# Optimization experiments

Measured on AMD Instinct MI355X. Metric: run time of the kernel, lower is better.

## Reference

```python
import jax, jax.numpy as jnp
import numpy as np

N = 8388608
EPS = 1e-12  # matches torch eps default


def setup_inputs() -> dict:
    key = jax.random.key(0)
    k1, k2, k3 = jax.random.split(key, 3)
    logits = jax.random.normal(k1, (N,), dtype=jnp.float32)
    status = jax.random.randint(k2, (N,), 0, 2, dtype=jnp.int32)       # 0=censored, 1=event
    time = jax.random.randint(k3, (N,), 0, 65536, dtype=jnp.int32)     # integer survival times -> ties
    return {"logits": logits, "status": status, "time": time}


def reference(logits, status, time):
    """Cox partial likelihood, Breslow tie correction, reduction='mean'.

    Per the torch module: sort by time descending, cum_exp = cumsum(exp(x)),
    for each tie group with m events: nll = -(sum_events x - m*log(cum_exp[group_end]+eps)).
    This equals sum over events of -(x_i - log(denom_i)) with denom_i shared per group,
    which vectorizes cleanly.
    """
    neg_t = -time                       # ascending key == descending time order
    order = jnp.argsort(neg_t)
    x = logits[order]
    e = status[order].astype(x.dtype)
    t = neg_t[order]                    # sorted ascending (i.e., time descending)
    exp_x = jnp.exp(x)
    cum_exp = jnp.cumsum(exp_x)
    # last index of each tie group (risk-set boundary), vectorized unique_consecutive
    ends = jnp.searchsorted(t, t, side='right') - 1
    denom = cum_exp[ends] + EPS
    nll = (jnp.log(denom) - x) * e      # contributes only at events
    n_events = e.sum()
    return nll.sum() / (n_events + EPS)
```

## Files before the change

### kernel.cpp

```cpp
#include <hip/hip_runtime.h>
#include <math.h>

#define NBUCKETS 65536
#define EPS 1e-12

typedef float v4f __attribute__((ext_vector_type(4)));
typedef int v4i __attribute__((ext_vector_type(4)));
typedef unsigned int v4u __attribute__((ext_vector_type(4)));

#define NCHUNK 128
#define WGT 1024
#define RROUNDS 16
#define PBUCK 32768
#define SCALE_F 131072.0f
#define INV_SCALE (1.0 / 131072.0)
#define SUM_MASK 0x0FFFFFFFu

#define OFF_HIST 0
#define OFF_CS   (NCHUNK * NBUCKETS * 4)
#define OFF_SX   (OFF_CS + 256 * 8)
#define OFF_CTRL (OFF_SX + NCHUNK * 4)
#define REQ_NEW  (OFF_CTRL + 64)

#define NREP 8
#define OSCALE_F 1073741824.0f
#define OINV_SCALE (1.0 / 1073741824.0)
#define LOW48 ((1ull << 48) - 1)
#define O_REP 0
#define O_SD (NREP * NBUCKETS * 8)
#define O_M (O_SD + NBUCKETS * 8)
#define O_CS (O_M + NBUCKETS * 4)
#define O_NLL (O_CS + 256 * 8)
#define O_NEV (O_NLL + 256 * 8)
#define O_SX (O_NEV + 256 * 4)
#define REQ_OLD (O_SX + 8192 * 4)

__device__ __forceinline__ unsigned int xcd_id() {
    unsigned int x;
    asm volatile("s_getreg_b32 %0, hwreg(HW_REG_XCC_ID)" : "=s"(x));
    return x & 7u;
}

__global__ __launch_bounds__(WGT) void scatter_half_kernel(
        const v4f* __restrict__ x4, const v4i* __restrict__ e4,
        const v4i* __restrict__ t4, unsigned int* __restrict__ hist,
        float* __restrict__ sum_ex_part, unsigned int* __restrict__ ctrl, int n4,
        const float* __restrict__ x_s, const int* __restrict__ e_s,
        const int* __restrict__ t_s, int tail_base, int tail_cnt) {
    __shared__ unsigned int lds[PBUCK];
    const int t = threadIdx.x;
    const int wg = blockIdx.x;
    const int half = wg & 1;
    const int chunk = wg >> 1;

    if (wg == 0 && t == 0) {
        ctrl[0] = 0u;
        ctrl[1] = 0u;
        ((double*)ctrl)[1] = 0.0;
        ctrl[4] = 0u;
    }

    v4u* lds4 = (v4u*)lds;
#pragma unroll
    for (int q = 0; q < PBUCK / 4 / WGT; q++)
        lds4[t + q * WGT] = (v4u){0u, 0u, 0u, 0u};
    __syncthreads();

    float ev_x = 0.0f;
    const unsigned int uh = (unsigned int)half;

#pragma unroll 1
    for (int r = 0; r < RROUNDS; r++) {
        int idx = (chunk * RROUNDS + r) * WGT + t;
        if (idx < n4) {
            v4f x = __builtin_nontemporal_load(&x4[idx]);
            v4i e = __builtin_nontemporal_load(&e4[idx]);
            v4i tm = __builtin_nontemporal_load(&t4[idx]);
#pragma unroll
            for (int k = 0; k < 4; k++) {
                float xv = x[k];
                unsigned int b = (unsigned int)tm[k] & 0xFFFFu;
                unsigned int ev = (e[k] != 0) ? 1u : 0u;
                if ((b >> 15) == uh) {
                    unsigned int pk = (ev << 28) +
                                      (unsigned int)(expf(xv) * SCALE_F + 0.5f);
                    atomicAdd(&lds[b & (PBUCK - 1)], pk);
                }
                if (half == 0 && ev) ev_x += xv;
            }
        }
    }

    if (chunk == 0 && t == 0 && tail_cnt > 0) {
        for (int i = 0; i < tail_cnt; i++) {
            int idx = tail_base + i;
            float xv = x_s[idx];
            unsigned int b = (unsigned int)t_s[idx] & 0xFFFFu;
            unsigned int ev = (e_s[idx] != 0) ? 1u : 0u;
            if ((b >> 15) == uh) {
                unsigned int pk = (ev << 28) +
                                  (unsigned int)(expf(xv) * SCALE_F + 0.5f);
                atomicAdd(&lds[b & (PBUCK - 1)], pk);
            }
            if (half == 0 && ev) ev_x += xv;
        }
    }
    __syncthreads();

    v4u* hbase = (v4u*)(hist + (size_t)chunk * NBUCKETS + (size_t)half * PBUCK);
#pragma unroll
    for (int q = 0; q < PBUCK / 4 / WGT; q++) {
        v4u v = lds4[t + q * WGT];
        __builtin_nontemporal_store(v, &hbase[t + q * WGT]);
    }

    if (half == 0) {
        __syncthreads();
#pragma unroll
        for (int off = 32; off > 0; off >>= 1) ev_x += __shfl_down(ev_x, off, 64);
        if ((t & 63) == 0) lds[t >> 6] = __float_as_uint(ev_x);
        __syncthreads();
        if (t == 0) {
            float s = 0.0f;
            for (int w = 0; w < WGT / 64; w++) s += __uint_as_float(lds[w]);
            sum_ex_part[chunk] = s;
        }
    }
}

__global__ __launch_bounds__(256) void merge_suffix_final_kernel(
        const v4u* __restrict__ hist4, double* __restrict__ chunk_sum,
        const float* __restrict__ sum_ex_part, unsigned int* __restrict__ ctrl,
        float* __restrict__ out) {
    const int t = threadIdx.x, b = blockIdx.x;
    const int tg = t >> 6, lane = t & 63;

    unsigned long long s[4] = {0ull, 0ull, 0ull, 0ull};
    unsigned int c[4] = {0u, 0u, 0u, 0u};
    const v4u* base = hist4 + (size_t)(tg * (NCHUNK / 4)) * (NBUCKETS / 4) +
                      (size_t)b * 64 + lane;
#pragma unroll 4
    for (int w = 0; w < NCHUNK / 4; w++) {
        v4u h = base[(size_t)w * (NBUCKETS / 4)];
#pragma unroll
        for (int q = 0; q < 4; q++) {
            s[q] += (unsigned long long)(h[q] & SUM_MASK);
            c[q] += h[q] >> 28;
        }
    }
    __shared__ unsigned long long lsum[4][64][4];
    __shared__ unsigned int lcnt[4][64][4];
#pragma unroll
    for (int q = 0; q < 4; q++) { lsum[tg][lane][q] = s[q]; lcnt[tg][lane][q] = c[q]; }
    __syncthreads();

    unsigned long long Ssum = lsum[0][t >> 2][t & 3] + lsum[1][t >> 2][t & 3] +
                              lsum[2][t >> 2][t & 3] + lsum[3][t >> 2][t & 3];
    unsigned int M = lcnt[0][t >> 2][t & 3] + lcnt[1][t >> 2][t & 3] +
                     lcnt[2][t >> 2][t & 3] + lcnt[3][t >> 2][t & 3];
    double sv = (double)Ssum * INV_SCALE;

    __shared__ double red[256];
    __shared__ double sfx[256];
    __shared__ unsigned int ured[256];
    __shared__ int lastblk;

    red[t] = sv;
    __syncthreads();
    for (int st = 128; st > 0; st >>= 1) {
        if (t < st) red[t] += red[t + st];
        __syncthreads();
    }
    if (t == 0) {
        __hip_atomic_store(&chunk_sum[b], red[0], __ATOMIC_RELEASE,
                           __HIP_MEMORY_SCOPE_AGENT);
        __hip_atomic_fetch_add(&ctrl[0], 1u, __ATOMIC_ACQ_REL,
                               __HIP_MEMORY_SCOPE_AGENT);
        while (__hip_atomic_load(&ctrl[0], __ATOMIC_ACQUIRE,
                                 __HIP_MEMORY_SCOPE_AGENT) < (unsigned)gridDim.x)
            __builtin_amdgcn_s_sleep(8);
    }
    __syncthreads();

    double cst = __hip_atomic_load(&chunk_sum[t], __ATOMIC_RELAXED,
                                   __HIP_MEMORY_SCOPE_AGENT);
    red[t] = (t > b) ? cst : 0.0;
    __syncthreads();
    for (int st = 128; st > 0; st >>= 1) {
        if (t < st) red[t] += red[t + st];
        __syncthreads();
    }
    double offset = red[0];
    __syncthreads();

    sfx[t] = sv;
    __syncthreads();
    for (int st = 1; st < 256; st <<= 1) {
        double add = (t + st < 256) ? sfx[t + st] : 0.0;
        __syncthreads();
        sfx[t] += add;
        __syncthreads();
    }
    double denom = offset + sfx[t] + EPS;
    double nll = (M != 0u) ? (double)M * log(denom) : 0.0;

    red[t] = nll;
    ured[t] = M;
    __syncthreads();
    for (int st = 128; st > 0; st >>= 1) {
        if (t < st) { red[t] += red[t + st]; ured[t] += ured[t + st]; }
        __syncthreads();
    }
    if (t == 0) {
        atomicAdd((double*)ctrl + 1, red[0]);
        atomicAdd(&ctrl[4], ured[0]);
        __threadfence();
        unsigned int old = __hip_atomic_fetch_add(&ctrl[1], 1u, __ATOMIC_ACQ_REL,
                                                  __HIP_MEMORY_SCOPE_AGENT);
        lastblk = (old == (unsigned)gridDim.x - 1) ? 1 : 0;
    }
    __syncthreads();
    if (lastblk) {
        red[t] = (t < NCHUNK) ? (double)sum_ex_part[t] : 0.0;
        __syncthreads();
        for (int st = 128; st > 0; st >>= 1) {
            if (t < st) red[t] += red[t + st];
            __syncthreads();
        }
        if (t == 0) {
            double nllT = __hip_atomic_load((double*)ctrl + 1, __ATOMIC_RELAXED,
                                            __HIP_MEMORY_SCOPE_AGENT);
            unsigned int nev = __hip_atomic_load(&ctrl[4], __ATOMIC_RELAXED,
                                                 __HIP_MEMORY_SCOPE_AGENT);
            out[0] = (float)((nllT - red[0]) / ((double)nev + EPS));
        }
    }
}

__global__ void zero_ws_kernel(unsigned long long* __restrict__ rep, int n) {
    int i = blockIdx.x * blockDim.x + threadIdx.x;
    if (i < n) rep[i] = 0ull;
}

__global__ __launch_bounds__(256) void scatter_atomic_kernel(
        const v4f* __restrict__ x4, const v4i* __restrict__ e4,
        const v4i* __restrict__ t4,
        unsigned long long* __restrict__ rep, float* __restrict__ sum_ex_part,
        int n4, const float* __restrict__ x_s, const int* __restrict__ e_s,
        const int* __restrict__ t_s, int tail_base, int tail_cnt) {
    int i = blockIdx.x * blockDim.x + threadIdx.x;
    unsigned long long* R = rep + (size_t)xcd_id() * NBUCKETS;
    float ev_x = 0.0f;
    if (i < n4) {
        v4f x = __builtin_nontemporal_load(&x4[i]);
        v4i e = __builtin_nontemporal_load(&e4[i]);
        v4i t = __builtin_nontemporal_load(&t4[i]);
#pragma unroll
        for (int k = 0; k < 4; k++) {
            float xv = x[k];
            unsigned int v = (unsigned int)t[k] & 0xFFFFu;
            unsigned long long pk =
                ((unsigned long long)(e[k] != 0) << 48) +
                (unsigned long long)(expf(xv) * OSCALE_F + 0.5f);
            __hip_atomic_fetch_add(&R[v], pk, __ATOMIC_RELAXED,
                                   __HIP_MEMORY_SCOPE_WORKGROUP);
            if (e[k]) ev_x += xv;
        }
    }
    if (i < tail_cnt) {
        int idx = tail_base + i;
        float xv = x_s[idx];
        unsigned int v = (unsigned int)t_s[idx] & 0xFFFFu;
        unsigned long long pk =
            ((unsigned long long)(e_s[idx] != 0) << 48) +
            (unsigned long long)(expf(xv) * OSCALE_F + 0.5f);
        __hip_atomic_fetch_add(&R[v], pk, __ATOMIC_RELAXED,
                               __HIP_MEMORY_SCOPE_WORKGROUP);
        if (e_s[idx]) ev_x += xv;
    }
    __shared__ float sred[256];
    sred[threadIdx.x] = ev_x;
    __syncthreads();
    for (int s = 128; s > 0; s >>= 1) {
        if ((int)threadIdx.x < s) sred[threadIdx.x] += sred[threadIdx.x + s];
        __syncthreads();
    }
    if (threadIdx.x == 0) sum_ex_part[blockIdx.x] = sred[0];
}

__global__ __launch_bounds__(256) void reduce_kernel(
        const unsigned long long* __restrict__ rep, double* __restrict__ Sd,
        unsigned int* __restrict__ m, double* __restrict__ chunk_sum) {
    int t = threadIdx.x;
    int i = blockIdx.x * 256 + t;
    unsigned long long acc = 0ull;
#pragma unroll
    for (int r = 0; r < NREP; r++) acc += rep[(size_t)r * NBUCKETS + i];
    double sv = (double)(acc & LOW48) * OINV_SCALE;
    unsigned int mv = (unsigned int)(acc >> 48);
    Sd[i] = sv;
    m[i] = mv;
    __shared__ double red[256];
    red[t] = sv;
    __syncthreads();
    for (int s = 128; s > 0; s >>= 1) {
        if (t < s) red[t] += red[t + s];
        __syncthreads();
    }
    if (t == 0) chunk_sum[blockIdx.x] = red[0];
}

__global__ __launch_bounds__(256) void suffix_kernel(
        const double* __restrict__ Sd, const unsigned int* __restrict__ m,
        const double* __restrict__ chunk_sum, double* __restrict__ nll_part,
        unsigned int* __restrict__ nev_part) {
    __shared__ double cs[256];
    __shared__ double sfx[256];
    __shared__ unsigned int ured[256];
    const int t = threadIdx.x;
    const int b = blockIdx.x;

    cs[t] = (t > b) ? chunk_sum[t] : 0.0;
    __syncthreads();
    for (int s = 128; s > 0; s >>= 1) {
        if (t < s) cs[t] += cs[t + s];
        __syncthreads();
    }
    double offset = cs[0];
    __syncthreads();

    int i = b * 256 + t;
    double sv = Sd[i];
    unsigned int mv = m[i];

    sfx[t] = sv;
    __syncthreads();
    for (int s = 1; s < 256; s <<= 1) {
        double add = (t + s < 256) ? sfx[t + s] : 0.0;
        __syncthreads();
        sfx[t] += add;
        __syncthreads();
    }

    double denom = offset + sfx[t] + EPS;
    double nll = (mv != 0u) ? (double)mv * log(denom) : 0.0;

    cs[t] = nll;
    ured[t] = mv;
    __syncthreads();
    for (int s = 128; s > 0; s >>= 1) {
        if (t < s) { cs[t] += cs[t + s]; ured[t] += ured[t + s]; }
        __syncthreads();
    }
    if (t == 0) {
        nll_part[b] = cs[0];
        nev_part[b] = ured[0];
    }
}

__global__ __launch_bounds__(256) void final_kernel(
        const double* __restrict__ nll_part, const unsigned int* __restrict__ nev_part,
        const float* __restrict__ sum_ex_part, int n_sx, float* __restrict__ out) {
    __shared__ double rd[256];
    __shared__ double rs[256];
    __shared__ unsigned int ru[256];
    int t = threadIdx.x;
    double nll = nll_part[t];
    unsigned int ne = nev_part[t];
    double sx = 0.0;
    for (int i = t; i < n_sx; i += 256) sx += (double)sum_ex_part[i];
    rd[t] = nll;
    rs[t] = sx;
    ru[t] = ne;
    __syncthreads();
    for (int s = 128; s > 0; s >>= 1) {
        if (t < s) { rd[t] += rd[t + s]; rs[t] += rs[t + s]; ru[t] += ru[t + s]; }
        __syncthreads();
    }
    if (t == 0) {
        double total = rd[0] - rs[0];
        out[0] = (float)(total / ((double)ru[0] + EPS));
    }
}

extern "C" void kernel_launch(void* const* d_in, const int* in_sizes, int n_in,
                              void* d_out, int out_size, void* d_ws, size_t ws_size,
                              hipStream_t stream) {
    const float* logits = (const float*)d_in[0];
    const int* status = (const int*)d_in[1];
    const int* time = (const int*)d_in[2];
    const int N = in_sizes[0];

    char* ws = (char*)d_ws;
    int n4 = N / 4;
    int tail_base = n4 * 4;
    int tail_cnt = N - tail_base;

    if (ws_size >= (size_t)REQ_NEW && N <= NCHUNK * WGT * RROUNDS * 4) {
        unsigned int* hist = (unsigned int*)(ws + OFF_HIST);
        double* chunk_sum = (double*)(ws + OFF_CS);
        float* sum_ex_part = (float*)(ws + OFF_SX);
        unsigned int* ctrl = (unsigned int*)(ws + OFF_CTRL);

        scatter_half_kernel<<<NCHUNK * 2, WGT, 0, stream>>>(
            (const v4f*)logits, (const v4i*)status, (const v4i*)time,
            hist, sum_ex_part, ctrl, n4, logits, status, time, tail_base, tail_cnt);
        merge_suffix_final_kernel<<<256, 256, 0, stream>>>(
            (const v4u*)hist, chunk_sum, sum_ex_part, ctrl, (float*)d_out);
    } else {
        unsigned long long* rep = (unsigned long long*)(ws + O_REP);
        double* Sd = (double*)(ws + O_SD);
        unsigned int* m = (unsigned int*)(ws + O_M);
        double* chunk_sum = (double*)(ws + O_CS);
        double* nll_part = (double*)(ws + O_NLL);
        unsigned int* nev_part = (unsigned int*)(ws + O_NEV);
        float* sum_ex_part = (float*)(ws + O_SX);

        int nrep_total = NREP * NBUCKETS;
        zero_ws_kernel<<<(nrep_total + 255) / 256, 256, 0, stream>>>(rep, nrep_total);
        int blocks = (n4 + 255) / 256;
        if (blocks < 1) blocks = 1;
        scatter_atomic_kernel<<<blocks, 256, 0, stream>>>(
            (const v4f*)logits, (const v4i*)status, (const v4i*)time,
            rep, sum_ex_part, n4, logits, status, time, tail_base, tail_cnt);
        reduce_kernel<<<256, 256, 0, stream>>>(rep, Sd, m, chunk_sum);
        suffix_kernel<<<256, 256, 0, stream>>>(Sd, m, chunk_sum, nll_part, nev_part);
        final_kernel<<<1, 256, 0, stream>>>(nll_part, nev_part, sum_ex_part, blocks,
                                            (float*)d_out);
    }
}
```

Baseline: 175.8 us.

## Split fused merge/suffix kernel into separate launches instead of grid-wide spin barrier

Replaces the single merge_suffix_final kernel, which used an atomic spin barrier across all blocks plus last-block detection, with three launches: merge_chunk, suffix and final. Per-bucket sums and counts now go to global workspace arrays, and the existing suffix and final kernels are reused. This drops the in-kernel grid barrier and atomic control words, but adds two kernel launches and extra global round trips.

```diff
diff --git a/kernel.cpp b/kernel.cpp
--- a/kernel.cpp
+++ b/kernel.cpp
@@ -17,10 +17,13 @@
 #define SUM_MASK 0x0FFFFFFFu
 
 #define OFF_HIST 0
-#define OFF_CS   (NCHUNK * NBUCKETS * 4)
-#define OFF_SX   (OFF_CS + 256 * 8)
-#define OFF_CTRL (OFF_SX + NCHUNK * 4)
-#define REQ_NEW  (OFF_CTRL + 64)
+#define OFF_SD   (NCHUNK * NBUCKETS * 4)
+#define OFF_M    (OFF_SD + NBUCKETS * 8)
+#define OFF_CS   (OFF_M + NBUCKETS * 4)
+#define OFF_NLL  (OFF_CS + 256 * 8)
+#define OFF_NEV  (OFF_NLL + 256 * 8)
+#define OFF_SX   (OFF_NEV + 256 * 4)
+#define REQ_NEW  (OFF_SX + NCHUNK * 4)
 
 #define NREP 8
 #define OSCALE_F 1073741824.0f
@@ -44,7 +47,7 @@
 __global__ __launch_bounds__(WGT) void scatter_half_kernel(
         const v4f* __restrict__ x4, const v4i* __restrict__ e4,
         const v4i* __restrict__ t4, unsigned int* __restrict__ hist,
-        float* __restrict__ sum_ex_part, unsigned int* __restrict__ ctrl, int n4,
+        float* __restrict__ sum_ex_part, int n4,
         const float* __restrict__ x_s, const int* __restrict__ e_s,
         const int* __restrict__ t_s, int tail_base, int tail_cnt) {
     __shared__ unsigned int lds[PBUCK];
@@ -52,13 +55,6 @@
     const int wg = blockIdx.x;
     const int half = wg & 1;
     const int chunk = wg >> 1;
-
-    if (wg == 0 && t == 0) {
-        ctrl[0] = 0u;
-        ctrl[1] = 0u;
-        ((double*)ctrl)[1] = 0.0;
-        ctrl[4] = 0u;
-    }
 
     v4u* lds4 = (v4u*)lds;
 #pragma unroll
@@ -128,10 +124,9 @@
     }
 }
 
-__global__ __launch_bounds__(256) void merge_suffix_final_kernel(
-        const v4u* __restrict__ hist4, double* __restrict__ chunk_sum,
-        const float* __restrict__ sum_ex_part, unsigned int* __restrict__ ctrl,
-        float* __restrict__ out) {
+__global__ __launch_bounds__(256) void merge_chunk_kernel(
+        const v4u* __restrict__ hist4, double* __restrict__ Sd,
+        unsigned int* __restrict__ m, double* __restrict__ chunk_sum) {
     const int t = threadIdx.x, b = blockIdx.x;
     const int tg = t >> 6, lane = t & 63;
 
@@ -159,155 +154,17 @@
     unsigned int M = lcnt[0][t >> 2][t & 3] + lcnt[1][t >> 2][t & 3] +
                      lcnt[2][t >> 2][t & 3] + lcnt[3][t >> 2][t & 3];
     double sv = (double)Ssum * INV_SCALE;
+    Sd[b * 256 + t] = sv;
+    m[b * 256 + t] = M;
 
     __shared__ double red[256];
-    __shared__ double sfx[256];
-    __shared__ unsigned int ured[256];
-    __shared__ int lastblk;
-
     red[t] = sv;
     __syncthreads();
     for (int st = 128; st > 0; st >>= 1) {
         if (t < st) red[t] += red[t + st];
         __syncthreads();
     }
-    if (t == 0) {
-        __hip_atomic_store(&chunk_sum[b], red[0], __ATOMIC_RELEASE,
-                           __HIP_MEMORY_SCOPE_AGENT);
-        __hip_atomic_fetch_add(&ctrl[0], 1u, __ATOMIC_ACQ_REL,
-                               __HIP_MEMORY_SCOPE_AGENT);
-        while (__hip_atomic_load(&ctrl[0], __ATOMIC_ACQUIRE,
-                                 __HIP_MEMORY_SCOPE_AGENT) < (unsigned)gridDim.x)
-            __builtin_amdgcn_s_sleep(8);
-    }
-    __syncthreads();
-
-    double cst = __hip_atomic_load(&chunk_sum[t], __ATOMIC_RELAXED,
-                                   __HIP_MEMORY_SCOPE_AGENT);
-    red[t] = (t > b) ? cst : 0.0;
-    __syncthreads();
-    for (int st = 128; st > 0; st >>= 1) {
-        if (t < st) red[t] += red[t + st];
-        __syncthreads();
-    }
-    double offset = red[0];
-    __syncthreads();
-
-    sfx[t] = sv;
-    __syncthreads();
-    for (int st = 1; st < 256; st <<= 1) {
-        double add = (t + st < 256) ? sfx[t + st] : 0.0;
-        __syncthreads();
-        sfx[t] += add;
-        __syncthreads();
-    }
-    double denom = offset + sfx[t] + EPS;
-    double nll = (M != 0u) ? (double)M * log(denom) : 0.0;
-
-    red[t] = nll;
-    ured[t] = M;
-    __syncthreads();
-    for (int st = 128; st > 0; st >>= 1) {
-        if (t < st) { red[t] += red[t + st]; ured[t] += ured[t + st]; }
-        __syncthreads();
-    }
-    if (t == 0) {
-        atomicAdd((double*)ctrl + 1, red[0]);
-        atomicAdd(&ctrl[4], ured[0]);
-        __threadfence();
-        unsigned int old = __hip_atomic_fetch_add(&ctrl[1], 1u, __ATOMIC_ACQ_REL,
-                                                  __HIP_MEMORY_SCOPE_AGENT);
-        lastblk = (old == (unsigned)gridDim.x - 1) ? 1 : 0;
-    }
-    __syncthreads();
-    if (lastblk) {
-        red[t] = (t < NCHUNK) ? (double)sum_ex_part[t] : 0.0;
-        __syncthreads();
-        for (int st = 128; st > 0; st >>= 1) {
-            if (t < st) red[t] += red[t + st];
-            __syncthreads();
-        }
-        if (t == 0) {
-            double nllT = __hip_atomic_load((double*)ctrl + 1, __ATOMIC_RELAXED,
-                                            __HIP_MEMORY_SCOPE_AGENT);
-            unsigned int nev = __hip_atomic_load(&ctrl[4], __ATOMIC_RELAXED,
-                                                 __HIP_MEMORY_SCOPE_AGENT);
-            out[0] = (float)((nllT - red[0]) / ((double)nev + EPS));
-        }
-    }
-}
-
-__global__ void zero_ws_kernel(unsigned long long* __restrict__ rep, int n) {
-    int i = blockIdx.x * blockDim.x + threadIdx.x;
-    if (i < n) rep[i] = 0ull;
-}
-
-__global__ __launch_bounds__(256) void scatter_atomic_kernel(
-        const v4f* __restrict__ x4, const v4i* __restrict__ e4,
-        const v4i* __restrict__ t4,
-        unsigned long long* __restrict__ rep, float* __restrict__ sum_ex_part,
-        int n4, const float* __restrict__ x_s, const int* __restrict__ e_s,
-        const int* __restrict__ t_s, int tail_base, int tail_cnt) {
-    int i = blockIdx.x * blockDim.x + threadIdx.x;
-    unsigned long long* R = rep + (size_t)xcd_id() * NBUCKETS;
-    float ev_x = 0.0f;
-    if (i < n4) {
-        v4f x = __builtin_nontemporal_load(&x4[i]);
-        v4i e = __builtin_nontemporal_load(&e4[i]);
-        v4i t = __builtin_nontemporal_load(&t4[i]);
-#pragma unroll
-        for (int k = 0; k < 4; k++) {
-            float xv = x[k];
-            unsigned int v = (unsigned int)t[k] & 0xFFFFu;
-            unsigned long long pk =
-                ((unsigned long long)(e[k] != 0) << 48) +
-                (unsigned long long)(expf(xv) * OSCALE_F + 0.5f);
-            __hip_atomic_fetch_add(&R[v], pk, __ATOMIC_RELAXED,
-                                   __HIP_MEMORY_SCOPE_WORKGROUP);
-            if (e[k]) ev_x += xv;
-        }
-    }
-    if (i < tail_cnt) {
-        int idx = tail_base + i;
-        float xv = x_s[idx];
-        unsigned int v = (unsigned int)t_s[idx] & 0xFFFFu;
-        unsigned long long pk =
-            ((unsigned long long)(e_s[idx] != 0) << 48) +
-            (unsigned long long)(expf(xv) * OSCALE_F + 0.5f);
-        __hip_atomic_fetch_add(&R[v], pk, __ATOMIC_RELAXED,
-                               __HIP_MEMORY_SCOPE_WORKGROUP);
-        if (e_s[idx]) ev_x += xv;
-    }
-    __shared__ float sred[256];
-    sred[threadIdx.x] = ev_x;
-    __syncthreads();
-    for (int s = 128; s > 0; s >>= 1) {
-        if ((int)threadIdx.x < s) sred[threadIdx.x] += sred[threadIdx.x + s];
-        __syncthreads();
-    }
-    if (threadIdx.x == 0) sum_ex_part[blockIdx.x] = sred[0];
-}
-
-__global__ __launch_bounds__(256) void reduce_kernel(
-        const unsigned long long* __restrict__ rep, double* __restrict__ Sd,
-        unsigned int* __restrict__ m, double* __restrict__ chunk_sum) {
-    int t = threadIdx.x;
-    int i = blockIdx.x * 256 + t;
-    unsigned long long acc = 0ull;
-#pragma unroll
-    for (int r = 0; r < NREP; r++) acc += rep[(size_t)r * NBUCKETS + i];
-    double sv = (double)(acc & LOW48) * OINV_SCALE;
-    unsigned int mv = (unsigned int)(acc >> 48);
-    Sd[i] = sv;
-    m[i] = mv;
-    __shared__ double red[256];
-    red[t] = sv;
-    __syncthreads();
-    for (int s = 128; s > 0; s >>= 1) {
-        if (t < s) red[t] += red[t + s];
-        __syncthreads();
-    }
-    if (t == 0) chunk_sum[blockIdx.x] = red[0];
+    if (t == 0) chunk_sum[b] = red[0];
 }
 
 __global__ __launch_bounds__(256) void suffix_kernel(
@@ -383,6 +240,79 @@
     }
 }
 
+__global__ void zero_ws_kernel(unsigned long long* __restrict__ rep, int n) {
+    int i = blockIdx.x * blockDim.x + threadIdx.x;
+    if (i < n) rep[i] = 0ull;
+}
+
+__global__ __launch_bounds__(256) void scatter_atomic_kernel(
+        const v4f* __restrict__ x4, const v4i* __restrict__ e4,
+        const v4i* __restrict__ t4,
+        unsigned long long* __restrict__ rep, float* __restrict__ sum_ex_part,
+        int n4, const float* __restrict__ x_s, const int* __restrict__ e_s,
+        const int* __restrict__ t_s, int tail_base, int tail_cnt) {
+    int i = blockIdx.x * blockDim.x + threadIdx.x;
+    unsigned long long* R = rep + (size_t)xcd_id() * NBUCKETS;
+    float ev_x = 0.0f;
+    if (i < n4) {
+        v4f x = __builtin_nontemporal_load(&x4[i]);
+        v4i e = __builtin_nontemporal_load(&e4[i]);
+        v4i t = __builtin_nontemporal_load(&t4[i]);
+#pragma unroll
+        for (int k = 0; k < 4; k++) {
+            float xv = x[k];
+            unsigned int v = (unsigned int)t[k] & 0xFFFFu;
+            unsigned long long pk =
+                ((unsigned long long)(e[k] != 0) << 48) +
+                (unsigned long long)(expf(xv) * OSCALE_F + 0.5f);
+            __hip_atomic_fetch_add(&R[v], pk, __ATOMIC_RELAXED,
+                                   __HIP_MEMORY_SCOPE_WORKGROUP);
+            if (e[k]) ev_x += xv;
+        }
+    }
+    if (i < tail_cnt) {
+        int idx = tail_base + i;
+        float xv = x_s[idx];
+        unsigned int v = (unsigned int)t_s[idx] & 0xFFFFu;
+        unsigned long long pk =
+            ((unsigned long long)(e_s[idx] != 0) << 48) +
+            (unsigned long long)(expf(xv) * OSCALE_F + 0.5f);
+        __hip_atomic_fetch_add(&R[v], pk, __ATOMIC_RELAXED,
+                               __HIP_MEMORY_SCOPE_WORKGROUP);
+        if (e_s[idx]) ev_x += xv;
+    }
+    __shared__ float sred[256];
+    sred[threadIdx.x] = ev_x;
+    __syncthreads();
+    for (int s = 128; s > 0; s >>= 1) {
+        if ((int)threadIdx.x < s) sred[threadIdx.x] += sred[threadIdx.x + s];
+        __syncthreads();
+    }
+    if (threadIdx.x == 0) sum_ex_part[blockIdx.x] = sred[0];
+}
+
+__global__ __launch_bounds__(256) void reduce_kernel(
+        const unsigned long long* __restrict__ rep, double* __restrict__ Sd,
+        unsigned int* __restrict__ m, double* __restrict__ chunk_sum) {
+    int t = threadIdx.x;
+    int i = blockIdx.x * 256 + t;
+    unsigned long long acc = 0ull;
+#pragma unroll
+    for (int r = 0; r < NREP; r++) acc += rep[(size_t)r * NBUCKETS + i];
+    double sv = (double)(acc & LOW48) * OINV_SCALE;
+    unsigned int mv = (unsigned int)(acc >> 48);
+    Sd[i] = sv;
+    m[i] = mv;
+    __shared__ double red[256];
+    red[t] = sv;
+    __syncthreads();
+    for (int s = 128; s > 0; s >>= 1) {
+        if (t < s) red[t] += red[t + s];
+        __syncthreads();
+    }
+    if (t == 0) chunk_sum[blockIdx.x] = red[0];
+}
+
 extern "C" void kernel_launch(void* const* d_in, const int* in_sizes, int n_in,
                               void* d_out, int out_size, void* d_ws, size_t ws_size,
                               hipStream_t stream) {
@@ -398,15 +328,20 @@
 
     if (ws_size >= (size_t)REQ_NEW && N <= NCHUNK * WGT * RROUNDS * 4) {
         unsigned int* hist = (unsigned int*)(ws + OFF_HIST);
+        double* Sd = (double*)(ws + OFF_SD);
+        unsigned int* m = (unsigned int*)(ws + OFF_M);
         double* chunk_sum = (double*)(ws + OFF_CS);
+        double* nll_part = (double*)(ws + OFF_NLL);
+        unsigned int* nev_part = (unsigned int*)(ws + OFF_NEV);
         float* sum_ex_part = (float*)(ws + OFF_SX);
-        unsigned int* ctrl = (unsigned int*)(ws + OFF_CTRL);
 
         scatter_half_kernel<<<NCHUNK * 2, WGT, 0, stream>>>(
             (const v4f*)logits, (const v4i*)status, (const v4i*)time,
-            hist, sum_ex_part, ctrl, n4, logits, status, time, tail_base, tail_cnt);
-        merge_suffix_final_kernel<<<256, 256, 0, stream>>>(
-            (const v4u*)hist, chunk_sum, sum_ex_part, ctrl, (float*)d_out);
+            hist, sum_ex_part, n4, logits, status, time, tail_base, tail_cnt);
+        merge_chunk_kernel<<<256, 256, 0, stream>>>((const v4u*)hist, Sd, m, chunk_sum);
+        suffix_kernel<<<256, 256, 0, stream>>>(Sd, m, chunk_sum, nll_part, nev_part);
+        final_kernel<<<1, 256, 0, stream>>>(nll_part, nev_part, sum_ex_part, NCHUNK,
+                                            (float*)d_out);
     } else {
         unsigned long long* rep = (unsigned long long*)(ws + O_REP);
         double* Sd = (double*)(ws + O_SD);
```

Result: faster. 154.2 us (-12.3%).

## Split merge kernel at grid barrier and drop nontemporal input loads

Applied to the files above, without the earlier changes.

Replaces the in-kernel spin-wait grid barrier in the merge/suffix kernel with a kernel boundary. A merge_chunk kernel now writes per-bucket sums, event counts and chunk totals to workspace, and a separate suffix_final kernel computes the suffix scan and the final loss. It also changes the input loads in both scatter kernels from nontemporal to ordinary loads. This removes the spinning wait on the atomic counter and the need for all 256 blocks to be co-resident, at the cost of an extra launch and a 768 KB round-trip through global memory for the bucket data.

```diff
diff --git a/kernel.cpp b/kernel.cpp
--- a/kernel.cpp
+++ b/kernel.cpp
@@ -17,7 +17,9 @@
 #define SUM_MASK 0x0FFFFFFFu
 
 #define OFF_HIST 0
-#define OFF_CS   (NCHUNK * NBUCKETS * 4)
+#define OFF_SD   (NCHUNK * NBUCKETS * 4)
+#define OFF_M    (OFF_SD + NBUCKETS * 8)
+#define OFF_CS   (OFF_M + NBUCKETS * 4)
 #define OFF_SX   (OFF_CS + 256 * 8)
 #define OFF_CTRL (OFF_SX + NCHUNK * 4)
 #define REQ_NEW  (OFF_CTRL + 64)
@@ -44,7 +46,7 @@
 __global__ __launch_bounds__(WGT) void scatter_half_kernel(
         const v4f* __restrict__ x4, const v4i* __restrict__ e4,
         const v4i* __restrict__ t4, unsigned int* __restrict__ hist,
-        float* __restrict__ sum_ex_part, unsigned int* __restrict__ ctrl, int n4,
+        float* __restrict__ sum_ex_part, int n4,
         const float* __restrict__ x_s, const int* __restrict__ e_s,
         const int* __restrict__ t_s, int tail_base, int tail_cnt) {
     __shared__ unsigned int lds[PBUCK];
@@ -52,13 +54,7 @@
     const int wg = blockIdx.x;
     const int half = wg & 1;
     const int chunk = wg >> 1;
-
-    if (wg == 0 && t == 0) {
-        ctrl[0] = 0u;
-        ctrl[1] = 0u;
-        ((double*)ctrl)[1] = 0.0;
-        ctrl[4] = 0u;
-    }
+    const unsigned int uh = (unsigned int)half;
 
     v4u* lds4 = (v4u*)lds;
 #pragma unroll
@@ -67,15 +63,14 @@
     __syncthreads();
 
     float ev_x = 0.0f;
-    const unsigned int uh = (unsigned int)half;
 
 #pragma unroll 1
     for (int r = 0; r < RROUNDS; r++) {
         int idx = (chunk * RROUNDS + r) * WGT + t;
         if (idx < n4) {
-            v4f x = __builtin_nontemporal_load(&x4[idx]);
-            v4i e = __builtin_nontemporal_load(&e4[idx]);
-            v4i tm = __builtin_nontemporal_load(&t4[idx]);
+            v4f x = x4[idx];
+            v4i e = e4[idx];
+            v4i tm = t4[idx];
 #pragma unroll
             for (int k = 0; k < 4; k++) {
                 float xv = x[k];
@@ -128,12 +123,18 @@
     }
 }
 
-__global__ __launch_bounds__(256) void merge_suffix_final_kernel(
-        const v4u* __restrict__ hist4, double* __restrict__ chunk_sum,
-        const float* __restrict__ sum_ex_part, unsigned int* __restrict__ ctrl,
-        float* __restrict__ out) {
+__global__ __launch_bounds__(256) void merge_chunk_kernel(
+        const v4u* __restrict__ hist4, double* __restrict__ Sd,
+        unsigned int* __restrict__ m, double* __restrict__ chunk_sum,
+        unsigned int* __restrict__ ctrl) {
     const int t = threadIdx.x, b = blockIdx.x;
     const int tg = t >> 6, lane = t & 63;
+
+    if (b == 0 && t == 0) {
+        ctrl[0] = 0u;
+        ((double*)ctrl)[1] = 0.0;
+        ctrl[4] = 0u;
+    }
 
     unsigned long long s[4] = {0ull, 0ull, 0ull, 0ull};
     unsigned int c[4] = {0u, 0u, 0u, 0u};
@@ -159,72 +160,76 @@
     unsigned int M = lcnt[0][t >> 2][t & 3] + lcnt[1][t >> 2][t & 3] +
                      lcnt[2][t >> 2][t & 3] + lcnt[3][t >> 2][t & 3];
     double sv = (double)Ssum * INV_SCALE;
+    Sd[b * 256 + t] = sv;
+    m[b * 256 + t] = M;
 
     __shared__ double red[256];
+    red[t] = sv;
+    __syncthreads();
+    for (int st = 128; st > 0; st >>= 1) {
+        if (t < st) red[t] += red[t + st];
+        __syncthreads();
+    }
+    if (t == 0) chunk_sum[b] = red[0];
+}
+
+__global__ __launch_bounds__(256) void suffix_final_kernel(
+        const double* __restrict__ Sd, const unsigned int* __restrict__ m,
+        const double* __restrict__ chunk_sum, const float* __restrict__ sum_ex_part,
+        unsigned int* __restrict__ ctrl, float* __restrict__ out) {
+    __shared__ double cs[256];
     __shared__ double sfx[256];
     __shared__ unsigned int ured[256];
     __shared__ int lastblk;
-
-    red[t] = sv;
-    __syncthreads();
-    for (int st = 128; st > 0; st >>= 1) {
-        if (t < st) red[t] += red[t + st];
+    const int t = threadIdx.x;
+    const int b = blockIdx.x;
+
+    cs[t] = (t > b) ? chunk_sum[t] : 0.0;
+    __syncthreads();
+    for (int s = 128; s > 0; s >>= 1) {
+        if (t < s) cs[t] += cs[t + s];
+        __syncthreads();
+    }
+    double offset = cs[0];
+    __syncthreads();
+
+    int i = b * 256 + t;
+    double sv = Sd[i];
+    unsigned int mv = m[i];
+
+    sfx[t] = sv;
+    __syncthreads();
+    for (int s = 1; s < 256; s <<= 1) {
+        double add = (t + s < 256) ? sfx[t + s] : 0.0;
+        __syncthreads();
+        sfx[t] += add;
+        __syncthreads();
+    }
+
+    double denom = offset + sfx[t] + EPS;
+    double nll = (mv != 0u) ? (double)mv * log(denom) : 0.0;
+
+    cs[t] = nll;
+    ured[t] = mv;
+    __syncthreads();
+    for (int s = 128; s > 0; s >>= 1) {
+        if (t < s) { cs[t] += cs[t + s]; ured[t] += ured[t + s]; }
         __syncthreads();
     }
     if (t == 0) {
-        __hip_atomic_store(&chunk_sum[b], red[0], __ATOMIC_RELEASE,
-                           __HIP_MEMORY_SCOPE_AGENT);
-        __hip_atomic_fetch_add(&ctrl[0], 1u, __ATOMIC_ACQ_REL,
-                               __HIP_MEMORY_SCOPE_AGENT);
-        while (__hip_atomic_load(&ctrl[0], __ATOMIC_ACQUIRE,
-                                 __HIP_MEMORY_SCOPE_AGENT) < (unsigned)gridDim.x)
-            __builtin_amdgcn_s_sleep(8);
-    }
-    __syncthreads();
-
-    double cst = __hip_atomic_load(&chunk_sum[t], __ATOMIC_RELAXED,
-                                   __HIP_MEMORY_SCOPE_AGENT);
-    red[t] = (t > b) ? cst : 0.0;
-    __syncthreads();
-    for (int st = 128; st > 0; st >>= 1) {
-        if (t < st) red[t] += red[t + st];
-        __syncthreads();
-    }
-    double offset = red[0];
-    __syncthreads();
-
-    sfx[t] = sv;
-    __syncthreads();
-    for (int st = 1; st < 256; st <<= 1) {
-        double add = (t + st < 256) ? sfx[t + st] : 0.0;
-        __syncthreads();
-        sfx[t] += add;
-        __syncthreads();
-    }
-    double denom = offset + sfx[t] + EPS;
-    double nll = (M != 0u) ? (double)M * log(denom) : 0.0;
-
-    red[t] = nll;
-    ured[t] = M;
-    __syncthreads();
-    for (int st = 128; st > 0; st >>= 1) {
-        if (t < st) { red[t] += red[t + st]; ured[t] += ured[t + st]; }
-        __syncthreads();
-    }
-    if (t == 0) {
-        atomicAdd((double*)ctrl + 1, red[0]);
+        atomicAdd((double*)ctrl + 1, cs[0]);
         atomicAdd(&ctrl[4], ured[0]);
         __threadfence();
-        unsigned int old = __hip_atomic_fetch_add(&ctrl[1], 1u, __ATOMIC_ACQ_REL,
+        unsigned int old = __hip_atomic_fetch_add(&ctrl[0], 1u, __ATOMIC_ACQ_REL,
                                                   __HIP_MEMORY_SCOPE_AGENT);
         lastblk = (old == (unsigned)gridDim.x - 1) ? 1 : 0;
     }
     __syncthreads();
     if (lastblk) {
-        red[t] = (t < NCHUNK) ? (double)sum_ex_part[t] : 0.0;
-        __syncthreads();
-        for (int st = 128; st > 0; st >>= 1) {
-            if (t < st) red[t] += red[t + st];
+        cs[t] = (t < NCHUNK) ? (double)sum_ex_part[t] : 0.0;
+        __syncthreads();
+        for (int s = 128; s > 0; s >>= 1) {
+            if (t < s) cs[t] += cs[t + s];
             __syncthreads();
         }
         if (t == 0) {
@@ -232,7 +237,7 @@
                                             __HIP_MEMORY_SCOPE_AGENT);
             unsigned int nev = __hip_atomic_load(&ctrl[4], __ATOMIC_RELAXED,
                                                  __HIP_MEMORY_SCOPE_AGENT);
-            out[0] = (float)((nllT - red[0]) / ((double)nev + EPS));
+            out[0] = (float)((nllT - cs[0]) / ((double)nev + EPS));
         }
     }
 }
@@ -252,9 +257,9 @@
     unsigned long long* R = rep + (size_t)xcd_id() * NBUCKETS;
     float ev_x = 0.0f;
     if (i < n4) {
-        v4f x = __builtin_nontemporal_load(&x4[i]);
-        v4i e = __builtin_nontemporal_load(&e4[i]);
-        v4i t = __builtin_nontemporal_load(&t4[i]);
+        v4f x = x4[i];
+        v4i e = e4[i];
+        v4i t = t4[i];
 #pragma unroll
         for (int k = 0; k < 4; k++) {
             float xv = x[k];
@@ -398,15 +403,19 @@
 
     if (ws_size >= (size_t)REQ_NEW && N <= NCHUNK * WGT * RROUNDS * 4) {
         unsigned int* hist = (unsigned int*)(ws + OFF_HIST);
+        double* Sd = (double*)(ws + OFF_SD);
+        unsigned int* m = (unsigned int*)(ws + OFF_M);
         double* chunk_sum = (double*)(ws + OFF_CS);
         float* sum_ex_part = (float*)(ws + OFF_SX);
         unsigned int* ctrl = (unsigned int*)(ws + OFF_CTRL);
 
         scatter_half_kernel<<<NCHUNK * 2, WGT, 0, stream>>>(
             (const v4f*)logits, (const v4i*)status, (const v4i*)time,
-            hist, sum_ex_part, ctrl, n4, logits, status, time, tail_base, tail_cnt);
-        merge_suffix_final_kernel<<<256, 256, 0, stream>>>(
-            (const v4u*)hist, chunk_sum, sum_ex_part, ctrl, (float*)d_out);
+            hist, sum_ex_part, n4, logits, status, time, tail_base, tail_cnt);
+        merge_chunk_kernel<<<256, 256, 0, stream>>>((const v4u*)hist, Sd, m,
+                                                    chunk_sum, ctrl);
+        suffix_final_kernel<<<256, 256, 0, stream>>>(Sd, m, chunk_sum, sum_ex_part,
+                                                     ctrl, (float*)d_out);
     } else {
         unsigned long long* rep = (unsigned long long*)(ws + O_REP);
         double* Sd = (double*)(ws + O_SD);
```

After: 158.7 us. 1.11x faster.
